# Performance work log

Hardware: AMD Instinct MI355X
Metric: run time of the kernel (lower is better)

Reference implementation:

```python
import jax, jax.numpy as jnp
import numpy as np

NE = 32          # n_events
S = 65536        # n_samples
FR = 128         # n_frames
SR = 22050       # samplerate
NRES = 1024      # n_resonances
IEXP = 8         # instr_expressivity
NEXP = 4         # noise_expressivity
NFILT = 64       # n_noise_filters
FSAMP = 512      # noise_filter_samples
NDEF = 64        # n_deformations
NNDEF = 32       # noise_deformations
NENV = 64        # n_envelopes
NDEC = 64        # n_decays
ENV_SMALL = 128  # Envelopes n_samples
ENV_FULL = 8192  # Envelopes full_size
NVERB = 16       # number of impulse responses


def interp_last(x, size):
    # linear interpolation along last axis (align_corners=True style)
    n = x.shape[-1]
    pos = jnp.linspace(0.0, n - 1.0, size)
    lo = jnp.floor(pos).astype(jnp.int32)
    hi = jnp.clip(lo + 1, 0, n - 1)
    w = (pos - lo).astype(x.dtype)
    return x[..., lo] * (1.0 - w) + x[..., hi] * w


def fft_convolve(a, b):
    # linear convolution via zero-padded FFT, keep first n samples
    n = a.shape[-1]
    A = jnp.fft.rfft(a, n=2 * n)
    B = jnp.fft.rfft(b, n=2 * n)
    return jnp.fft.irfft(A * B, n=2 * n)[..., :n]


def select_items(sel, items):
    # softmax-weighted soft lookup over item bank
    return jax.nn.softmax(sel, axis=-1) @ items


def make_waves(n_samples, n_res, sr):
    freqs = np.linspace(20.0, 4000.0, num=n_res // 4)
    t = np.arange(n_samples, dtype=np.float64) / sr
    ph = freqs[:, None] * t[None, :]               # cycles
    sine = np.sin(2 * np.pi * ph)
    saw = 2.0 * (ph % 1.0) - 1.0
    square = np.sign(sine)
    tri = 2.0 * np.abs(saw) - 1.0
    w = np.concatenate([sine, saw, square, tri], axis=0)  # (n_res, n_samples)
    return jnp.asarray(w, dtype=jnp.float32)


def setup_inputs() -> dict:
    key = jax.random.key(0)
    ks = jax.random.split(key, 16)
    u = lambda k, shp: jax.random.uniform(k, shp, minval=-0.02, maxval=0.02, dtype=jnp.float32)
    inp = {
        'res_sel': jax.random.normal(ks[0], (1, NE, IEXP, NRES), jnp.float32),
        'noise_sel': jax.random.normal(ks[1], (1, NE, NEXP, NFILT), jnp.float32),
        'env_sel': jax.random.normal(ks[2], (1, NE, NENV), jnp.float32),
        'dec_sel': jax.random.normal(ks[3], (1, NE, 1, NDEC), jnp.float32),
        'def_sel': jax.random.normal(ks[4], (1, NE, NDEF), jnp.float32),
        'noise_def_sel': jax.random.normal(ks[5], (1, NE, NNDEF), jnp.float32),
        'mix_sel': jax.random.normal(ks[6], (1, NE, 2), jnp.float32),
        'room_sel': jax.random.normal(ks[7], (1, NE, NVERB), jnp.float32),
        'amp': jax.random.uniform(ks[8], (1, NE, 1), dtype=jnp.float32),
        # learned item banks (uniform(-0.02, 0.02) init as in Lookup)
        'r_items': u(ks[9], (NRES, NRES)),
        'n_items': u(ks[10], (NFILT, FSAMP)),
        'e_items': u(ks[11], (NENV, ENV_SMALL)),
        'd_items': u(ks[12], (NDEC, 1)),
        'warp_items': u(ks[13], (NDEF, IEXP * FR)),
        'nwarp_items': u(ks[14], (NNDEF, NEXP * FR)),
        # fixed buffers
        'verbs': jax.random.normal(ks[15], (NVERB, S), jnp.float32) * 0.01,
        'waves': make_waves(S, NRES, SR),
    }
    return inp


def reference(res_sel, noise_sel, env_sel, dec_sel, def_sel, noise_def_sel,
              mix_sel, room_sel, amp, r_items, n_items, e_items, d_items,
              warp_items, nwarp_items, verbs, waves):
    # --- Envelopes: items**2, soft lookup, upsample, multiply by noise, pad ---
    env = select_items(env_sel, e_items ** 2)            # (1, NE, 128)
    env = interp_last(env, ENV_FULL)                     # (1, NE, 8192)
    noise = jax.random.uniform(jax.random.key(42), env.shape,
                               minval=-1.0, maxval=1.0, dtype=env.dtype)
    env = env * noise
    impulses = jnp.pad(env, ((0, 0), (0, 0), (0, S - ENV_FULL)))  # (1, NE, S)

    # --- SampleLookup (windowed noise filters) ---
    k = jnp.arange(FSAMP, dtype=jnp.float32)
    hamming = 0.54 - 0.46 * jnp.cos(2.0 * jnp.pi * k / (FSAMP - 1))
    nfil = select_items(noise_sel, n_items * hamming)    # (1, NE, NEXP, FSAMP)
    nfil = jnp.pad(nfil, ((0, 0), (0, 0), (0, 0), (0, S - FSAMP)))
    filt = fft_convolve(impulses[:, :, None, :], nfil)   # (1, NE, NEXP, S)

    # --- noise Deformations: softmax over channel dim, upsample ---
    nd = select_items(noise_def_sel, nwarp_items)        # (1, NE, NEXP*FR)
    nd = nd.reshape(1, NE, NEXP, FR)
    nd = jax.nn.softmax(nd, axis=2)
    nd = interp_last(nd, S)                              # (1, NE, NEXP, S)
    filtered = (filt * nd).sum(axis=2)                   # (1, NE, S)

    # --- WavetableLookup resonances ---
    res = select_items(res_sel, r_items) @ waves         # (1, NE, IEXP, S)

    # --- Decays: log-domain cumsum -> exponential envelopes ---
    d_pre = 0.5 + jax.nn.sigmoid(d_items) * 0.5          # base_resonance=0.5
    d = select_items(dec_sel, d_pre)                     # (1, NE, 1, 1)
    d = jnp.tile(d, (1, 1, 1, FR))                       # (1, NE, 1, FR)
    d = jnp.exp(jnp.cumsum(jnp.log(d + 1e-12), axis=-1))
    d = interp_last(d, S)                                # (1, NE, 1, S)

    # --- instrument Deformations ---
    w = select_items(def_sel, warp_items)                # (1, NE, IEXP*FR)
    w = w.reshape(1, NE, IEXP, FR)
    w = jax.nn.softmax(w, axis=2)
    w = interp_last(w, S)                                # (1, NE, IEXP, S)

    dres = (res * d * w).sum(axis=2)                     # (1, NE, S)

    # --- excite resonances with filtered noise, add reverb, mix ---
    conv = fft_convolve(filtered, dres)                  # (1, NE, S)
    rooms = select_items(room_sel, verbs)                # (1, NE, S)
    wet = fft_convolve(conv, rooms)
    m = jax.nn.softmax(mix_sel, axis=-1)                 # (1, NE, 2)
    mixed = m[..., 0:1] * conv + m[..., 1:2] * wet
    return mixed * (amp ** 2)                            # (1, NE, S)
```

## Files before the change

### kernel.cpp

```cpp
#include <hip/hip_runtime.h>
#include <math.h>

#define NEV    32
#define NS     65536
#define NFFT   131072
#define ENVS   128
#define ENVF   8192
#define FSAMP2 512
#define NEXP2  4
#define FLEN   8704
#define GD     5622750u
#define GDH    2811375u

enum : size_t {
  O_ENV_SMALL = 0,
  O_NFIL      = 4096,
  O_IMP       = 69632,
  O_ND        = 331776,
  O_WSM       = 348160,
  O_DSM       = 380928,
  O_SCAL      = 385024,
  O_RHO       = 385152,
  O_P1        = 385664,
  O_P2        = 647808,
// ... 275 lines not shown
    Ahi[base + (size_t)(mg*8 + r)*8] = f2bf(acc[r]);
}

__global__ __launch_bounds__(64) void prep_kernel(
    const float* __restrict__ noise_sel, const float* __restrict__ env_sel,
    const float* __restrict__ dec_sel,   const float* __restrict__ def_sel,
    const float* __restrict__ ndef_sel,  const float* __restrict__ mix_sel,
    const float* __restrict__ room_sel,  const float* __restrict__ amp,
    const float* __restrict__ n_items,   const float* __restrict__ e_items,
    const float* __restrict__ d_items,   const float* __restrict__ warp_items,
    const float* __restrict__ nwarp_items,
    float* __restrict__ env_small, float* __restrict__ nfil,
    float* __restrict__ nd_small,  float* __restrict__ w_small,
    float* __restrict__ d_small,   float* __restrict__ scal,
    float* __restrict__ rho)
{
  const int e = blockIdx.x;
  const int l = threadIdx.x;
  __shared__ float sw[64];
  __shared__ float buf[1024];

  {
    float x = env_sel[e*64 + l];
    float mx = wmax(x);
    float ex = expf(x - mx);
    float sm = wsum(ex);
    sw[l] = ex / sm;
  }
  __syncthreads();
  #pragma unroll
  for (int c = 0; c < 2; c++){
    int j = l + 64*c;
    float acc = 0.f;
    for (int k = 0; k < 64; k++){ float it = e_items[k*ENVS + j]; acc += sw[k]*(it*it); }
    env_small[e*ENVS + j] = acc;
  }
  __syncthreads();

  for (int x = 0; x < NEXP2; x++){
    float v = noise_sel[(e*NEXP2 + x)*64 + l];
    float mxv = wmax(v);
    float exv = expf(v - mxv);
    float smv = wsum(exv);
    sw[l] = exv / smv;
    __syncthreads();
    for (int c = 0; c < 8; c++){
      int tau = l + 64*c;
      float acc = 0.f;
      for (int f = 0; f < 64; f++) acc += sw[f]*n_items[f*FSAMP2 + tau];
      float ham = 0.54f - 0.46f*cosf((6.2831853071795864769f * (float)tau) / 511.0f);
      nfil[(e*NEXP2 + x)*FSAMP2 + tau] = acc*ham;
    }
    __syncthreads();
  }

  {
    float x = def_sel[e*64 + l];
    float mx = wmax(x);
    float ex = expf(x - mx);
    float sm = wsum(ex);
    sw[l] = ex / sm;
  }
  __syncthreads();
  for (int c = 0; c < 16; c++){
    int idx = l + 64*c;
    float acc = 0.f;
    for (int k = 0; k < 64; k++) acc += sw[k]*warp_items[k*1024 + idx];
    buf[idx] = acc;
  }
  __syncthreads();
  #pragma unroll
  for (int c = 0; c < 2; c++){
    int f = l + 64*c;
    float mx = -1e30f;
    for (int i = 0; i < 8; i++) mx = fmaxf(mx, buf[i*128 + f]);
    float ev[8]; float s = 0.f;
    for (int i = 0; i < 8; i++){ ev[i] = expf(buf[i*128 + f] - mx); s += ev[i]; }
    for (int i = 0; i < 8; i++) w_small[(e*8 + i)*128 + f] = ev[i]/s;
  }
  __syncthreads();

  {
    float x = (l < 32) ? ndef_sel[e*32 + l] : -1e30f;
    float mx = wmax(x);
    float ex = (l < 32) ? expf(x - mx) : 0.f;
    float sm = wsum(ex);
    sw[l] = (l < 32) ? ex/sm : 0.f;
  }
  __syncthreads();
  for (int c = 0; c < 8; c++){
    int idx = l + 64*c;
    float acc = 0.f;
    for (int k = 0; k < 32; k++) acc += sw[k]*nwarp_items[k*512 + idx];
    buf[idx] = acc;
  }
  __syncthreads();
  #pragma unroll
  for (int c = 0; c < 2; c++){
    int j = l + 64*c;
    float mx = -1e30f;
    for (int x = 0; x < 4; x++) mx = fmaxf(mx, buf[x*128 + j]);
    float ev[4]; float s = 0.f;
    for (int x = 0; x < 4; x++){ ev[x] = expf(buf[x*128 + j] - mx); s += ev[x]; }
    for (int x = 0; x < 4; x++) nd_small[(e*4 + x)*128 + j] = ev[x]/s;
  }
  __syncthreads();

  {
    float x = dec_sel[e*64 + l];
    float mx = wmax(x);
    float ex = expf(x - mx);
    float sm = wsum(ex);
    float wgt = ex / sm;
    float di = d_items[l];
    float dp = 0.5f + 0.5f*(1.0f/(1.0f + expf(-di)));
    float d0 = wsum(wgt*dp);
    float ld = logf(d0 + 1e-12f);
    #pragma unroll
    for (int c = 0; c < 2; c++){
      int f = l + 64*c;
      d_small[e*128 + f] = expf((float)(f+1)*ld);
    }
  }
  if (l == 0){
    float a = mix_sel[e*2 + 0], b = mix_sel[e*2 + 1];
    float mm = fmaxf(a, b);
    float ea = expf(a - mm), eb = expf(b - mm);
    float ss = ea + eb;
    scal[e*4 + 0] = ea/ss;
    scal[e*4 + 1] = eb/ss;
    float am = amp[e];
    scal[e*4 + 2] = am*am;
  }
  {
    float x = (l < 16) ? room_sel[e*16 + l] : -1e30f;
    float mx = wmax(x);
    float ex = (l < 16) ? expf(x - mx) : 0.f;
    float sm = wsum(ex);
    if (l < 16) rho[e*16 + l] = ex/sm;
  }
}

__global__ __launch_bounds__(256) void p1_softmax_kernel(
    const float* __restrict__ res_sel, float* __restrict__ P1)
{
  const int m = blockIdx.x;
  const int tid = threadIdx.x;
  __shared__ float red[4], red2[4];
  const float* row = res_sel + (size_t)m*1024;
  float4 v = ((const float4*)row)[tid];
  float mx = fmaxf(fmaxf(v.x, v.y), fmaxf(v.z, v.w));
  #pragma unroll
  for (int o = 32; o > 0; o >>= 1) mx = fmaxf(mx, __shfl_xor(mx, o));
  if ((tid & 63) == 0) red[tid >> 6] = mx;
  __syncthreads();
  mx = fmaxf(fmaxf(red[0], red[1]), fmaxf(red[2], red[3]));
  float e0 = expf(v.x - mx), e1 = expf(v.y - mx), e2 = expf(v.z - mx), e3 = expf(v.w - mx);
  float s = e0 + e1 + e2 + e3;
  #pragma unroll
  for (int o = 32; o > 0; o >>= 1) s += __shfl_xor(s, o);
  if ((tid & 63) == 0) red2[tid >> 6] = s;
  __syncthreads();
  s = red2[0] + red2[1] + red2[2] + red2[3];
  float inv = 1.0f/s;
  ((float4*)(P1 + (size_t)m*1024))[tid] = make_float4(e0*inv, e1*inv, e2*inv, e3*inv);
}

__global__ __launch_bounds__(256) void p2_kernel(
    const float* __restrict__ P1, const float* __restrict__ r_items,
    float* __restrict__ P2)
{
  __shared__ __align__(16) float sp1[8][1024];
  const int bx = blockIdx.x;
  const int mg = blockIdx.y;
  const int tid = threadIdx.x;
  for (int idx = tid; idx < 2048; idx += 256)
    ((float4*)&sp1[0][0])[idx] = ((const float4*)(P1 + (size_t)mg*8*1024))[idx];
  __syncthreads();
  const int n = bx*256 + tid;
  float acc[8] = {0,0,0,0,0,0,0,0};
  for (int k = 0; k < 1024; k++){
    float wv = r_items[(size_t)k*1024 + n];
    #pragma unroll
    for (int r = 0; r < 8; r++) acc[r] += sp1[r][k]*wv;
  }
  #pragma unroll
  for (int r = 0; r < 8; r++) P2[(size_t)(mg*8 + r)*1024 + n] = acc[r];
}

__global__ __launch_bounds__(256) void env_noise_kernel(
    const float* __restrict__ env_small, float* __restrict__ impulses)
{
  const int flat = blockIdx.x*256 + threadIdx.x;
  const int e = flat >> 13, i = flat & 8191;
  unsigned bits = threefry_bits(0u, (unsigned)flat);
  float u01 = __uint_as_float((bits >> 9) | 0x3f800000u) - 1.0f;
  float nz  = fmaxf(-1.0f, u01*2.0f - 1.0f);
  float pos = (float)i * (127.0f/8191.0f);
  int lo = (int)floorf(pos);
  int hi = imin(lo + 1, 127);
  float w = pos - (float)lo;
  const float* es = env_small + e*ENVS;
  float v = es[lo]*(1.0f - w) + es[hi]*w;
  impulses[flat] = v*nz;
}

__global__ __launch_bounds__(256) void filt_kernel(
    const float* __restrict__ nfil, const float* __restrict__ impulses,
    const float* __restrict__ nd_small, float* __restrict__ filtered)
{
  __shared__ float nf[4*512];
  __shared__ float imp[768];
  const int e = blockIdx.y, t0 = blockIdx.x*256, tid = threadIdx.x;
  for (int idx = tid; idx < 2048; idx += 256) nf[idx] = nfil[e*2048 + idx];
  for (int idx = tid; idx < 768; idx += 256){
    int g = t0 - 512 + idx;
    imp[idx] = (g >= 0 && g < ENVF) ? impulses[e*ENVF + g] : 0.f;
  }
  __syncthreads();
  const int t = t0 + tid;
  float s0 = 0.f, s1 = 0.f, s2 = 0.f, s3 = 0.f;
  for (int tau = 0; tau < 512; tau++){
    float iv = imp[512 + tid - tau];
    s0 += nf[0*512 + tau]*iv;
    s1 += nf[1*512 + tau]*iv;
    s2 += nf[2*512 + tau]*iv;
    s3 += nf[3*512 + tau]*iv;
  }
  float pos = (float)t * (127.0f/65535.0f);
  int lo = (int)floorf(pos);
  int hi = imin(lo + 1, 127);
  float w = pos - (float)lo;
  const float* nds = nd_small + e*512;
  float acc = 0.f;
  acc += s0*(nds[0*128 + lo]*(1.0f - w) + nds[0*128 + hi]*w);
  acc += s1*(nds[1*128 + lo]*(1.0f - w) + nds[1*128 + hi]*w);
  acc += s2*(nds[2*128 + lo]*(1.0f - w) + nds[2*128 + hi]*w);
  acc += s3*(nds[3*128 + lo]*(1.0f - w) + nds[3*128 + hi]*w);
  filtered[e*FLEN + t] = acc;
}

__global__ __launch_bounds__(256) void rooms_kernel(
    const float* __restrict__ verbs, const float* __restrict__ rho,
    float* __restrict__ rooms)
{
  const int t = blockIdx.x*256 + threadIdx.x;
  const int e = blockIdx.y;
  float acc = 0.f;
  #pragma unroll
  for (int v = 0; v < 16; v++) acc += rho[e*16 + v]*verbs[(size_t)v*NS + t];
  rooms[(size_t)e*NS + t] = acc;
}

__device__ __noinline__ float slow_wave(int wf, int n, int i){
  const double stp = 3980.0 / 255.0;
  double fi = (i == 255) ? 4000.0 : __dadd_rn(__dmul_rn((double)i, stp), 20.0);
  double tn = (double)n / 22050.0;
  double ph = __dmul_rn(fi, tn);
  double fr = ph - trunc(ph);
  if (wf == 1) return (float)(2.0*fr - 1.0);
  if (wf == 3){ double sw = 2.0*fr - 1.0; return (float)(2.0*fabs(sw) - 1.0); }
  if (fr == 0.0 || fr == 0.5){
    if (ph == 0.0) return 0.0f;
    double sv = sin(__dmul_rn(6.283185307179586, ph));
    return (sv > 0.0) ? 1.0f : ((sv < 0.0) ? -1.0f : 0.0f);
  }
  return (fr < 0.5) ? 1.0f : -1.0f;
}

__device__ __forceinline__ void gen8(int wf, int n, int i0,
                                     unsigned m_in, unsigned stepn,
                                     U8& bh, U8& bl)
{
  unsigned m = m_in;
  #pragma unroll
  for (int j = 0; j < 8; j++){
    float fr = (float)m * (1.0f/5622750.0f);
    float val;
    bool rare;
    if (wf == 0){
      asm("v_sin_f32 %0, %1" : "=v"(val) : "v"(fr));
      rare = false;
    } else if (wf == 1){
      val = fmaf(fr, 2.0f, -1.0f);
      rare = (m == 0u);
    } else if (wf == 2){
      val = (m < GDH) ? 1.0f : -1.0f;
      rare = (m == 0u) || (m == GDH);
    } else {
      val = fmaf(fabsf(fmaf(fr, 2.0f, -1.0f)), 2.0f, -1.0f);
      rare = (m == 0u);
    }
    if (rare) val = slow_wave(wf, n, i0 + j);
    unsigned ub = __float_as_uint(val);
    unsigned th = ub & 0xFFFF0000u;
    float lres = val - __uint_as_float(th);
    bh.u[j] = (unsigned short)(ub >> 16);
    bl.u[j] = (unsigned short)(__float_as_uint(lres) >> 16);
    m += stepn;
    if (m >= GD) m -= GD;
  }
}

__global__ __launch_bounds__(512, 2) void gemm_dres_gen3_kernel(
    const unsigned short* __restrict__ Ahi,
    const float* __restrict__ w_small, const float* __restrict__ d_small,
    float* __restrict__ dres)
{
  __shared__ __align__(16) unsigned short Abuf[2][8192];

  const int tid = threadIdx.x;
  const int l = tid & 63, w = tid >> 6;
  const int g = l >> 4, c = l & 15;
  const int n = blockIdx.x*128 + w*16 + c;

  f32x4 acc[16];
  #pragma unroll
  for (int m = 0; m < 16; m++) acc[m] = (f32x4){0.f,0.f,0.f,0.f};

  const unsigned stepn = (3980u*(unsigned)n) % GD;
  const unsigned s32 = (32u*stepn) % GD;
  const unsigned K0g = 3980u*(unsigned)(g*8) + 5100u;
  const unsigned m0 = (unsigned)(((unsigned long long)(unsigned)n * K0g) % GD);
  unsigned mseg = m0;

  typedef const __attribute__((address_space(1))) void GV;
  typedef __attribute__((address_space(3))) void LV;

  #pragma unroll
  for (int q = 0; q < 2; q++){
    const unsigned short* src = Ahi + (size_t)q*4096 + (size_t)w*512 + (size_t)l*8;
    __builtin_amdgcn_global_load_lds((GV*)src, (LV*)&Abuf[0][q*4096 + w*512], 16, 0, 0);
  }
  __syncthreads();

  for (int k0 = 0; k0 < 1024; k0 += 32){
    const int cur = (k0 >> 5) & 1, nxt = cur ^ 1;
    const int wf = k0 >> 8;
    if ((k0 & 255) == 0) mseg = m0;

    if (k0 + 32 < 1024){
      const size_t slice = (size_t)((k0 + 32) >> 5) * 8192;
      #pragma unroll
      for (int q = 0; q < 2; q++){
        const unsigned short* src = Ahi + slice + (size_t)q*4096 + (size_t)w*512 + (size_t)l*8;
        __builtin_amdgcn_global_load_lds((GV*)src, (LV*)&Abuf[nxt][q*4096 + w*512], 16, 0, 0);
      }
    }

    const int i0 = (k0 & 255) + g*8;
    U8 bh, bl;
    gen8(wf, n, i0, mseg, stepn, bh, bl);
    mseg += s32; if (mseg >= GD) mseg -= GD;

    #pragma unroll
    for (int m = 0; m < 16; m++){
      U8 ah;
      ah.q = *(const uint4*)&Abuf[cur][g*2048 + (m*16 + c)*8];
      acc[m] = __builtin_amdgcn_mfma_f32_16x16x32_bf16(ah.v, bh.v, acc[m], 0, 0, 0);
      acc[m] = __builtin_amdgcn_mfma_f32_16x16x32_bf16(ah.v, bl.v, acc[m], 0, 0, 0);
    }
    __syncthreads();
  }

  const int t = n;
  float pos = (float)t * (127.0f/65535.0f);
  int lo = (int)floorf(pos);
  int hi = imin(lo + 1, 127);
  float fr = pos - (float)lo;
  #pragma unroll
  for (int m = 0; m < 16; m++){
    int e = 2*m + (g >> 1);
    float s = 0.f;
    #pragma unroll
    for (int jj = 0; jj < 4; jj++){
      int i = (g & 1)*4 + jj;
      const float* wr = w_small + (size_t)(e*8 + i)*128;
      float wi = wr[lo]*(1.0f - fr) + wr[hi]*fr;
      s += wi * acc[m][jj];
    }
    s += __shfl_xor(s, 16);
    if ((g & 1) == 0){
      float de = d_small[e*128 + lo]*(1.0f - fr) + d_small[e*128 + hi]*fr;
      dres[(size_t)e*NS + t] = de * s;
    }
  }
}

__global__ __launch_bounds__(256) void gemm_dres_kernel(
    const float* __restrict__ P2, const float* __restrict__ waves,
    const float* __restrict__ w_small, const float* __restrict__ d_small,
    float* __restrict__ dres)
{
  __shared__ __align__(16) float At[32][256];
  __shared__ __align__(16) float Bt[32][64];
  const int tid = threadIdx.x;
  const int tx = tid & 15, ty = tid >> 4;
  const int n0 = blockIdx.x * 64;
  float acc[16][4];
  #pragma unroll
  for (int a = 0; a < 16; a++)
    #pragma unroll
    for (int b = 0; b < 4; b++) acc[a][b] = 0.f;

  for (int k0 = 0; k0 < 1024; k0 += 32){
    {
      const float4* src = (const float4*)(P2 + (size_t)tid*1024 + k0);
      #pragma unroll
      for (int q = 0; q < 8; q++){
        float4 v = src[q];
        At[q*4 + 0][tid] = v.x; At[q*4 + 1][tid] = v.y;
        At[q*4 + 2][tid] = v.z; At[q*4 + 3][tid] = v.w;
      }
    }
    {
      int c  = tid & 15;
      int kr = tid >> 4;
      *(float4*)&Bt[kr][c*4]      = *((const float4*)(waves + (size_t)(k0 + kr)*NS + n0) + c);
      *(float4*)&Bt[kr + 16][c*4] = *((const float4*)(waves + (size_t)(k0 + kr + 16)*NS + n0) + c);
    }
    __syncthreads();
    #pragma unroll 4
    for (int k = 0; k < 32; k++){
      float a[16];
      *(float4*)&a[0]  = *(const float4*)&At[k][ty*16 + 0];
      *(float4*)&a[4]  = *(const float4*)&At[k][ty*16 + 4];
      *(float4*)&a[8]  = *(const float4*)&At[k][ty*16 + 8];
      *(float4*)&a[12] = *(const float4*)&At[k][ty*16 + 12];
      float4 b = *(const float4*)&Bt[k][tx*4];
      #pragma unroll
      for (int mi = 0; mi < 16; mi++){
        acc[mi][0] += a[mi]*b.x;
        acc[mi][1] += a[mi]*b.y;
        acc[mi][2] += a[mi]*b.z;
        acc[mi][3] += a[mi]*b.w;
      }
    }
    __syncthreads();
  }

  #pragma unroll
  for (int ni = 0; ni < 4; ni++){
    int t = n0 + tx*4 + ni;
    float pos = (float)t * (127.0f/65535.0f);
    int lo = (int)floorf(pos);
    int hi = imin(lo + 1, 127);
    float w = pos - (float)lo;
    #pragma unroll
    for (int ev2 = 0; ev2 < 2; ev2++){
      int e = ty*2 + ev2;
      float de = d_small[e*128 + lo]*(1.0f - w) + d_small[e*128 + hi]*w;
      float s = 0.f;
      #pragma unroll
      for (int i = 0; i < 8; i++){
        const float* wrow = w_small + (size_t)(e*8 + i)*128;
        float wi = wrow[lo]*(1.0f - w) + wrow[hi]*w;
        s += wi * acc[ev2*8 + i][ni];
      }
      dres[(size_t)e*NS + t] = de * s;
    }
  }
}


template<int L, int Ns, int DIR>
__device__ __forceinline__ void r4_stage(const float* __restrict__ xr,
                                         const float* __restrict__ xi,
                                         float* __restrict__ yr,
                                         float* __restrict__ yi)
{
  const int tid = threadIdx.x;
  constexpr int BPR = L/4;
  #pragma unroll
  for (int q = 0; q < 4; q++){
    int bf = tid + 256*q;
    int r  = bf / BPR;
    int j  = bf % BPR;
    int sw = (r & 7) << 2;
    int jm = j & (Ns - 1);
    float2 w1 = twid((float)jm * (1.0f/(4.0f*(float)Ns)));
    if (DIR < 0) w1.y = -w1.y;
    float2 w2 = make_float2(w1.x*w1.x - w1.y*w1.y, 2.0f*w1.x*w1.y);
    float2 w3 = make_float2(w2.x*w1.x - w2.y*w1.y, w2.x*w1.y + w2.y*w1.x);
    const float* xrr = xr + r*L;
    const float* xir = xi + r*L;
    float ar  = xrr[j ^ sw],           ai  = xir[j ^ sw];
    float b0r = xrr[(j+BPR) ^ sw],     b0i = xir[(j+BPR) ^ sw];
    float c0r = xrr[(j+2*BPR) ^ sw],   c0i = xir[(j+2*BPR) ^ sw];
    float d0r = xrr[(j+3*BPR) ^ sw],   d0i = xir[(j+3*BPR) ^ sw];
    float br = b0r*w1.x - b0i*w1.y,  bi = b0r*w1.y + b0i*w1.x;
    float cr = c0r*w2.x - c0i*w2.y,  ci = c0r*w2.y + c0i*w2.x;
    float dr = d0r*w3.x - d0i*w3.y,  di = d0r*w3.y + d0i*w3.x;
    float apc_r = ar + cr, apc_i = ai + ci;
    float amc_r = ar - cr, amc_i = ai - ci;
    float bpd_r = br + dr, bpd_i = bi + di;
    float bmd_r = br - dr, bmd_i = bi - di;
    int dbase = ((j - jm) << 2) + jm;
    float* yrr = yr + r*L;
    float* yir = yi + r*L;
    yrr[dbase ^ sw]          = apc_r + bpd_r;
    yir[dbase ^ sw]          = apc_i + bpd_i;
    yrr[(dbase + 2*Ns) ^ sw] = apc_r - bpd_r;
    yir[(dbase + 2*Ns) ^ sw] = apc_i - bpd_i;
    if (DIR > 0){
      yrr[(dbase + Ns) ^ sw]   = amc_r + bmd_i;
      yir[(dbase + Ns) ^ sw]   = amc_i - bmd_r;
      yrr[(dbase + 3*Ns) ^ sw] = amc_r - bmd_i;
      yir[(dbase + 3*Ns) ^ sw] = amc_i + bmd_r;
    } else {
      yrr[(dbase + Ns) ^ sw]   = amc_r - bmd_i;
      yir[(dbase + Ns) ^ sw]   = amc_i + bmd_r;
      yrr[(dbase + 3*Ns) ^ sw] = amc_r + bmd_i;
      yir[(dbase + 3*Ns) ^ sw] = amc_i - bmd_r;
    }
  }
}

#define FFT_SWAP { float* t_; t_=ra;ra=rb;rb=t_; t_=ia;ia=ib;ib=t_; }

template<int L, int DIR>
__device__ __forceinline__ void fft_core4(float*& ra, float*& ia, float*& rb, float*& ib)
{
  const int tid = threadIdx.x;
  if (L == 512){
    __syncthreads();
    #pragma unroll
    for (int q = 0; q < 8; q++){
      int bf = tid + 256*q;
      int r = bf >> 8, j = bf & 255;
      int sw = (r & 7) << 2;
      float ar = ra[r*512 + (j ^ sw)],        ai = ia[r*512 + (j ^ sw)];
      float br = ra[r*512 + ((j+256) ^ sw)],  bi = ia[r*512 + ((j+256) ^ sw)];
      rb[r*512 + ((2*j) ^ sw)]   = ar + br;
      ib[r*512 + ((2*j) ^ sw)]   = ai + bi;
      rb[r*512 + ((2*j+1) ^ sw)] = ar - br;
      ib[r*512 + ((2*j+1) ^ sw)] = ai - bi;
    }
    FFT_SWAP
    __syncthreads(); r4_stage<512,   2, DIR>(ra, ia, rb, ib); FFT_SWAP
    __syncthreads(); r4_stage<512,   8, DIR>(ra, ia, rb, ib); FFT_SWAP
    __syncthreads(); r4_stage<512,  32, DIR>(ra, ia, rb, ib); FFT_SWAP
    __syncthreads(); r4_stage<512, 128, DIR>(ra, ia, rb, ib); FFT_SWAP
  } else {
    __syncthreads(); r4_stage<256,   1, DIR>(ra, ia, rb, ib); FFT_SWAP
    __syncthreads(); r4_stage<256,   4, DIR>(ra, ia, rb, ib); FFT_SWAP
    __syncthreads(); r4_stage<256,  16, DIR>(ra, ia, rb, ib); FFT_SWAP
    __syncthreads(); r4_stage<256,  64, DIR>(ra, ia, rb, ib); FFT_SWAP
  }
  __syncthreads();
}

__global__ __launch_bounds__(256) void fwd512_all_kernel(
    const float* __restrict__ filt, const float* __restrict__ dresv,
    const float* __restrict__ verbs, const float* __restrict__ rho,
    float2* __restrict__ Xf, float2* __restrict__ Xd, float2* __restrict__ Xr)
{
  __shared__ float reA[4096], imA[4096], reB[4096], imB[4096];
  __shared__ float srho[32];
  const int e = blockIdx.y, t1 = blockIdx.x*8, tid = threadIdx.x;
  const int z = blockIdx.z;
  if (z == 2){
    if (tid < 32) srho[tid] = rho[(2*e)*16 + tid];
    __syncthreads();
  }
  #pragma unroll
  for (int q = 0; q < 4; q++){
    int flat = tid + 256*q;
    int n2 = flat >> 1;
    int rb = (flat & 1)*4;
    int nb = t1 + rb + 256*n2;
    float4 va = make_float4(0.f,0.f,0.f,0.f);
    float4 vb = make_float4(0.f,0.f,0.f,0.f);
    if (z == 0){
      if (nb < FLEN){
        va = *(const float4*)(filt + (size_t)e*2*FLEN + nb);
        vb = *(const float4*)(filt + (size_t)e*2*FLEN + FLEN + nb);
      }
    } else if (z == 1){
      if (nb < NS){
        va = *(const float4*)(dresv + (size_t)e*2*NS + nb);
        vb = *(const float4*)(dresv + (size_t)e*2*NS + NS + nb);
      }
    } else {
      if (nb < NS){
        #pragma unroll
        for (int v = 0; v < 16; v++){
          float4 w4 = *(const float4*)(verbs + (size_t)v*NS + nb);
          float r0 = srho[v], r1 = srho[16 + v];
          va.x += r0*w4.x; va.y += r0*w4.y; va.z += r0*w4.z; va.w += r0*w4.w;
          vb.x += r1*w4.x; vb.y += r1*w4.y; vb.z += r1*w4.z; vb.w += r1*w4.w;
        }
      }
    }
    #pragma unroll
    for (int j = 0; j < 4; j++){
      int r = rb + j;
      int sw = (r & 7) << 2;
      reA[r*512 + (n2 ^ sw)] = (&va.x)[j];
      imA[r*512 + (n2 ^ sw)] = (&vb.x)[j];
    }
  }
  float *ra = reA, *ia = imA, *rb2 = reB, *ib2 = imB;
  fft_core4<512, +1>(ra, ia, rb2, ib2);
  float2* Bt = (z == 0) ? Xf : (z == 1) ? Xd : Xr;
  float2* dst = Bt + ((size_t)e << 17);
  #pragma unroll
  for (int q = 0; q < 16; q++){
    int idx = tid + 256*q;
    int r = idx & 7, k2 = idx >> 3;
    int n1 = t1 + r;
    int sw = (r & 7) << 2;
    float xr = ra[r*512 + (k2 ^ sw)];
    float xi = ia[r*512 + (k2 ^ sw)];
    float2 w = twid((float)(n1*k2) * (1.0f/131072.0f));
    dst[k2*256 + n1] = make_float2(xr*w.x - xi*w.y, xr*w.y + xi*w.x);
  }
}

__device__ __forceinline__ void fwd256_body(float2* __restrict__ S)
{
  __shared__ float reA[4096], imA[4096], reB[4096], imB[4096];
  const int e = blockIdx.y, K0 = blockIdx.x*16, tid = threadIdx.x;
  float2* base = S + ((size_t)e << 17) + (size_t)K0*256;
  #pragma unroll
  for (int q = 0; q < 16; q++){
    int idx = tid + 256*q;
    int r = idx >> 8, col = idx & 255;
    float2 v = base[r*256 + col];
    int sw = (r & 7) << 2;
    reA[r*256 + (col ^ sw)] = v.x;
    imA[r*256 + (col ^ sw)] = v.y;
  }
  float *ra = reA, *ia = imA, *rb = reB, *ib = imB;
  fft_core4<256, +1>(ra, ia, rb, ib);
  #pragma unroll
  for (int q = 0; q < 16; q++){
    int idx = tid + 256*q;
    int r = idx >> 8, col = idx & 255;
    int sw = (r & 7) << 2;
    base[r*256 + col] = make_float2(ra[r*256 + (col ^ sw)], ia[r*256 + (col ^ sw)]);
  }
}

__global__ __launch_bounds__(256) void fwd256_tri_kernel(
    float2* __restrict__ Xf, float2* __restrict__ Xd, float2* __restrict__ Xr)
{
  float2* S = (blockIdx.z == 0) ? Xf : (blockIdx.z == 1) ? Xd : Xr;
  fwd256_body(S);
}

__global__ __launch_bounds__(256) void fwd256_kernel(float2* __restrict__ S)
{
  fwd256_body(S);
}

__global__ __launch_bounds__(256) void inv256_mul2_kernel(
    const float2* __restrict__ ZA, const float2* __restrict__ ZB,
    float2* __restrict__ Ut)
{
  __shared__ float reA[4096], imA[4096], reB[4096], imB[4096];
  const int e = blockIdx.y, K0 = blockIdx.x*16, tid = threadIdx.x;
  const float2* Za = ZA + ((size_t)e << 17);
  const float2* Zb = ZB + ((size_t)e << 17);
  #pragma unroll
  for (int q = 0; q < 16; q++){
    int idx = tid + 256*q;
    int r = idx >> 8, col = idx & 255;
    int k2 = K0 + r;
    int k2p, k1p;
    if (k2 == 0){ k2p = 0; k1p = (256 - col) & 255; }
    else        { k2p = 512 - k2; k1p = 255 - col; }
    float2 za  = Za[(size_t)k2*256 + col];
    float2 zap = Za[(size_t)k2p*256 + k1p];
    float2 zb  = Zb[(size_t)k2*256 + col];
    float2 zbp = Zb[(size_t)k2p*256 + k1p];
    float a0r = 0.5f*(za.x + zap.x), a0i = 0.5f*(za.y - zap.y);
    float a1r = 0.5f*(za.y + zap.y), a1i = 0.5f*(zap.x - za.x);
    float b0r = 0.5f*(zb.x + zbp.x), b0i = 0.5f*(zb.y - zbp.y);
    float b1r = 0.5f*(zb.y + zbp.y), b1i = 0.5f*(zbp.x - zb.x);
    float p0r = a0r*b0r - a0i*b0i, p0i = a0r*b0i + a0i*b0r;
    float p1r = a1r*b1r - a1i*b1i, p1i = a1r*b1i + a1i*b1r;
    int sw = (r & 7) << 2;
    reA[r*256 + (col ^ sw)] = p0r - p1i;
    imA[r*256 + (col ^ sw)] = p0i + p1r;
  }
  float *ra = reA, *ia = imA, *rb = reB, *ib = imB;
  fft_core4<256, -1>(ra, ia, rb, ib);
  float2* dst = Ut + ((size_t)e << 17);
  #pragma unroll
  for (int q = 0; q < 16; q++){
    int idx = tid + 256*q;
    int r = idx & 15, n1 = idx >> 4;
    int k2 = K0 + r;
    int sw = (r & 7) << 2;
    float xr = ra[r*256 + (n1 ^ sw)];
    float xi = ia[r*256 + (n1 ^ sw)];
    float2 w = twid((float)(n1*k2) * (1.0f/131072.0f));
    dst[n1*512 + k2] = make_float2(xr*w.x + xi*w.y, xi*w.x - xr*w.y);
  }
}

__global__ __launch_bounds__(256) void inv512_fwdpack2_kernel(
    const float2* __restrict__ Ut, float* __restrict__ conv,
    float2* __restrict__ Bt)
{
  __shared__ float reA[4096], imA[4096], reB[4096], imB[4096];
  const int e = blockIdx.y, t1 = blockIdx.x*8, tid = threadIdx.x;
  const float2* base = Ut + ((size_t)e << 17) + (size_t)t1*512;
  #pragma unroll
  for (int q = 0; q < 16; q++){
    int idx = tid + 256*q;
    int r = idx >> 9, col = idx & 511;
    float2 v = base[r*512 + col];
    int sw = (r & 7) << 2;
    reA[r*512 + (col ^ sw)] = v.x;
    imA[r*512 + (col ^ sw)] = v.y;
  }
  float *ra = reA, *ia = imA, *rb = reB, *ib = imB;
  fft_core4<512, -1>(ra, ia, rb, ib);
  const float s = 1.0f/131072.0f;
  #pragma unroll
  for (int q = 0; q < 16; q++){
    int idx = tid + 256*q;
    int r = idx & 7, n2 = idx >> 3;
    int sw = (r & 7) << 2;
    int pos = r*512 + (n2 ^ sw);
    if (n2 < 256){
      int n = (t1 + r) + 256*n2;
      float y0 = ra[pos]*s, y1 = ia[pos]*s;
      conv[(size_t)(2*e)*NS + n]     = y0;
      conv[(size_t)(2*e + 1)*NS + n] = y1;
      rb[pos] = y0; ib[pos] = y1;
    } else {
      rb[pos] = 0.f; ib[pos] = 0.f;
    }
  }
  __syncthreads();
  float *r2 = rb, *i2 = ib, *r3 = ra, *i3 = ia;
  fft_core4<512, +1>(r2, i2, r3, i3);
  float2* dst = Bt + ((size_t)e << 17);
  #pragma unroll
  for (int q = 0; q < 16; q++){
    int idx = tid + 256*q;
    int r = idx & 7, k2 = idx >> 3;
    int n1 = t1 + r;
    int sw = (r & 7) << 2;
    float xr = r2[r*512 + (k2 ^ sw)];
    float xi = i2[r*512 + (k2 ^ sw)];
    float2 w = twid((float)(n1*k2) * (1.0f/131072.0f));
    dst[k2*256 + n1] = make_float2(xr*w.x - xi*w.y, xr*w.y + xi*w.x);
  }
}

__global__ __launch_bounds__(256) void inv512_mix2_kernel(
    const float2* __restrict__ Ut, const float* __restrict__ conv,
    const float* __restrict__ scal, float* __restrict__ dst)
{
  __shared__ float reA[4096], imA[4096], reB[4096], imB[4096];
  const int e = blockIdx.y, t1 = blockIdx.x*8, tid = threadIdx.x;
  const float2* base = Ut + ((size_t)e << 17) + (size_t)t1*512;
  #pragma unroll
  for (int q = 0; q < 16; q++){
    int idx = tid + 256*q;
    int r = idx >> 9, col = idx & 511;
    float2 v = base[r*512 + col];
    int sw = (r & 7) << 2;
    reA[r*512 + (col ^ sw)] = v.x;
    imA[r*512 + (col ^ sw)] = v.y;
  }
  float *ra = reA, *ia = imA, *rb = reB, *ib = imB;
  fft_core4<512, -1>(ra, ia, rb, ib);
  const float s = 1.0f/131072.0f;
  const int e0 = 2*e, e1 = 2*e + 1;
  float m00 = scal[e0*4 + 0], m10 = scal[e0*4 + 1], a20 = scal[e0*4 + 2];
  float m01 = scal[e1*4 + 0], m11 = scal[e1*4 + 1], a21 = scal[e1*4 + 2];
  #pragma unroll
  for (int q = 0; q < 8; q++){
    int idx = tid + 256*q;
    int r = idx & 7, n2 = idx >> 3;
    int n = (t1 + r) + 256*n2;
    int sw = (r & 7) << 2;
    int pos = r*512 + (n2 ^ sw);
    float w0 = ra[pos]*s, w1 = ia[pos]*s;
    size_t g0 = (size_t)e0*NS + n, g1 = (size_t)e1*NS + n;
    dst[g0] = (m00*conv[g0] + m10*w0)*a20;
    dst[g1] = (m01*conv[g1] + m11*w1)*a21;
  }
}

template<int MODE>
__global__ __launch_bounds__(256) void tconv_kernel(
    const float* __restrict__ sig, int sig_len, int sig_stride,
    const float* __restrict__ go, const float* __restrict__ scal,
    float* __restrict__ dst)
{
  __shared__ __align__(16) float cs[2048];
  __shared__ __align__(16) float rs[4104];
  const int e = blockIdx.y;
  const int t0 = blockIdx.x * 2048;
  const int tid = threadIdx.x;
  const int tb = tid * 8;
  float acc[8] = {0,0,0,0,0,0,0,0};
  const int kcap = imin(sig_len, t0 + 2048);
  for (int c0 = 0; c0 < kcap; c0 += 2048){
    __syncthreads();
    for (int idx = tid; idx < 2048; idx += 256){
      int gsi = c0 + idx;
      cs[idx] = (gsi < sig_len) ? sig[(size_t)e*sig_stride + gsi] : 0.f;
    }
    const int rb = t0 - c0 - 2056;
    for (int idx = tid; idx < 4104; idx += 256){
      int g = rb + idx;
      rs[idx] = (g >= 0 && g < NS) ? go[(size_t)e*NS + g] : 0.f;
    }
    __syncthreads();
    float W[12];
    int P = tb + 2056;
    *(float4*)&W[0] = *(const float4*)&rs[P - 4];
    *(float4*)&W[4] = *(const float4*)&rs[P];
    *(float4*)&W[8] = *(const float4*)&rs[P + 4];
    for (int u = 0; u < 512; u++){
      float4 f4 = *(const float4*)&cs[4*u];
      #pragma unroll
      for (int j = 0; j < 8; j++){
        acc[j] += f4.x*W[4 + j];
        acc[j] += f4.y*W[3 + j];
        acc[j] += f4.z*W[2 + j];
        acc[j] += f4.w*W[1 + j];
      }
      #pragma unroll
      for (int x2 = 11; x2 >= 4; x2--) W[x2] = W[x2 - 4];
      P -= 4;
      *(float4*)&W[0] = *(const float4*)&rs[P - 4];
    }
  }
  if (MODE == 0){
    #pragma unroll
    for (int j = 0; j < 8; j++) dst[(size_t)e*NS + t0 + tb + j] = acc[j];
  } else {
    float m0 = scal[e*4 + 0], m1 = scal[e*4 + 1], a2 = scal[e*4 + 2];
    #pragma unroll
    for (int j = 0; j < 8; j++){
      size_t gi = (size_t)e*NS + t0 + tb + j;
      dst[gi] = (m0*sig[gi] + m1*acc[j]) * a2;
    }
  }
}

extern "C" void kernel_launch(void* const* d_in, const int* in_sizes, int n_in,
                              void* d_out, int out_size, void* d_ws, size_t ws_size,
                              hipStream_t stream)
{
  (void)in_sizes; (void)n_in; (void)out_size;
  const float* res_sel     = (const float*)d_in[0];
  const float* noise_sel   = (const float*)d_in[1];
  const float* env_sel     = (const float*)d_in[2];
  const float* dec_sel     = (const float*)d_in[3];
  const float* def_sel     = (const float*)d_in[4];
  const float* ndef_sel    = (const float*)d_in[5];
  const float* mix_sel     = (const float*)d_in[6];
  const float* room_sel    = (const float*)d_in[7];
  const float* amp         = (const float*)d_in[8];
  const float* r_items     = (const float*)d_in[9];
  const float* n_items     = (const float*)d_in[10];
  const float* e_items     = (const float*)d_in[11];
  const float* d_items     = (const float*)d_in[12];
  const float* warp_items  = (const float*)d_in[13];
  const float* nwarp_items = (const float*)d_in[14];
  const float* verbs       = (const float*)d_in[15];
  const float* waves       = (const float*)d_in[16];
  float* ws  = (float*)d_ws;
  float* out = (float*)d_out;

  const bool big_ws = ws_size >= (size_t)O_END * sizeof(float);

  if (big_ws) {
    weights_kernel<<<dim3(NEV), dim3(64), 0, stream>>>(
        noise_sel, env_sel, dec_sel, def_sel, ndef_sel, mix_sel, room_sel, amp,
        d_items, ws + O_SWE, ws + O_SWN, ws + O_SWD, ws + O_SWND,
        ws + O_DSM, ws + O_SCAL, ws + O_RHO);
    lookups_kernel<<<dim3(224), dim3(256), 0, stream>>>(
        ws + O_SWE, ws + O_SWN, ws + O_SWD, ws + O_SWND,
        e_items, n_items, warp_items, nwarp_items,
        ws + O_ENV_SMALL, ws + O_NFIL, ws + O_WSM, ws + O_ND);

    unsigned short* Ahi = (unsigned short*)(ws + O_X);
    p2s_kernel<<<dim3(4, 32), dim3(256), 0, stream>>>(res_sel, r_items, Ahi);

    env_noise_kernel<<<dim3(1024), dim3(256), 0, stream>>>(ws + O_ENV_SMALL, ws + O_IMP);
    filt_kernel<<<dim3(34, NEV), dim3(256), 0, stream>>>(ws + O_NFIL, ws + O_IMP, ws + O_ND, ws + O_FILT);

    gemm_dres_gen3_kernel<<<dim3(512), dim3(512), 0, stream>>>(
        Ahi, ws + O_WSM, ws + O_DSM, ws + O_DRES);

    float2* Xf = (float2*)(ws + O_X);
    float2* Xd = (float2*)(ws + O_X + 4194304);
    float2* Xr = (float2*)(ws + O_Y);
    float2* Uc = (float2*)(ws + O_Y + 4194304);
    float2* Xc = Xf;
    float2* Uw = Xd;

    fwd512_all_kernel<<<dim3(32, 16, 3), dim3(256), 0, stream>>>(
        ws + O_FILT, ws + O_DRES, verbs, ws + O_RHO, Xf, Xd, Xr);
    fwd256_tri_kernel<<<dim3(32, 16, 3), dim3(256), 0, stream>>>(Xf, Xd, Xr);

    inv256_mul2_kernel<<<dim3(32, 16), dim3(256), 0, stream>>>(Xf, Xd, Uc);
    inv512_fwdpack2_kernel<<<dim3(32, 16), dim3(256), 0, stream>>>(Uc, ws + O_CONV, Xc);
    fwd256_kernel<<<dim3(32, 16), dim3(256), 0, stream>>>(Xc);
    inv256_mul2_kernel<<<dim3(32, 16), dim3(256), 0, stream>>>(Xc, Xr, Uw);
    inv512_mix2_kernel<<<dim3(32, 16), dim3(256), 0, stream>>>(
        Uw, ws + O_CONV, ws + O_SCAL, out);
  } else {
    prep_kernel<<<dim3(NEV), dim3(64), 0, stream>>>(
        noise_sel, env_sel, dec_sel, def_sel, ndef_sel, mix_sel, room_sel, amp,
        n_items, e_items, d_items, warp_items, nwarp_items,
        ws + O_ENV_SMALL, ws + O_NFIL, ws + O_ND, ws + O_WSM,
        ws + O_DSM, ws + O_SCAL, ws + O_RHO);
    p1_softmax_kernel<<<dim3(256), dim3(256), 0, stream>>>(res_sel, ws + O_P1);
    p2_kernel<<<dim3(4, 32), dim3(256), 0, stream>>>(ws + O_P1, r_items, ws + O_P2);
    env_noise_kernel<<<dim3(1024), dim3(256), 0, stream>>>(ws + O_ENV_SMALL, ws + O_IMP);
    filt_kernel<<<dim3(34, NEV), dim3(256), 0, stream>>>(ws + O_NFIL, ws + O_IMP, ws + O_ND, ws + O_FILT);
    rooms_kernel<<<dim3(256, NEV), dim3(256), 0, stream>>>(verbs, ws + O_RHO, ws + O_ROOMS);
    gemm_dres_kernel<<<dim3(1024), dim3(256), 0, stream>>>(
        ws + O_P2, waves, ws + O_WSM, ws + O_DSM, ws + O_DRES);
    tconv_kernel<0><<<dim3(32, NEV), dim3(256), 0, stream>>>(
        ws + O_FILT, FLEN, FLEN, ws + O_DRES, (const float*)nullptr, ws + O_CONV);
    tconv_kernel<1><<<dim3(32, NEV), dim3(256), 0, stream>>>(
        ws + O_CONV, NS, NS, ws + O_ROOMS, ws + O_SCAL, out);
  }
}
```

Baseline: 356.2 us.

## Fold dry/wet mix into spectral multiply and double GEMM K-step per stage

```diff
diff --git a/kernel.cpp b/kernel.cpp
--- a/kernel.cpp
+++ b/kernel.cpp
@@ -601,12 +601,12 @@
   }
 }
 
-__global__ __launch_bounds__(512, 2) void gemm_dres_gen3_kernel(
+__global__ __launch_bounds__(512, 2) void gemm_dres_gen4_kernel(
     const unsigned short* __restrict__ Ahi,
     const float* __restrict__ w_small, const float* __restrict__ d_small,
     float* __restrict__ dres)
 {
-  __shared__ __align__(16) unsigned short Abuf[2][8192];
+  __shared__ __align__(16) unsigned short Abuf[2][16384];
 
   const int tid = threadIdx.x;
   const int l = tid & 63, w = tid >> 6;
@@ -627,37 +627,40 @@
   typedef __attribute__((address_space(3))) void LV;
 
   #pragma unroll
-  for (int q = 0; q < 2; q++){
+  for (int q = 0; q < 4; q++){
     const unsigned short* src = Ahi + (size_t)q*4096 + (size_t)w*512 + (size_t)l*8;
     __builtin_amdgcn_global_load_lds((GV*)src, (LV*)&Abuf[0][q*4096 + w*512], 16, 0, 0);
   }
   __syncthreads();
 
-  for (int k0 = 0; k0 < 1024; k0 += 32){
-    const int cur = (k0 >> 5) & 1, nxt = cur ^ 1;
+  for (int k0 = 0; k0 < 1024; k0 += 64){
+    const int cur = (k0 >> 6) & 1, nxt = cur ^ 1;
     const int wf = k0 >> 8;
     if ((k0 & 255) == 0) mseg = m0;
 
-    if (k0 + 32 < 1024){
-      const size_t slice = (size_t)((k0 + 32) >> 5) * 8192;
+    if (k0 + 64 < 1024){
+      const size_t sb = (size_t)((k0 + 64) >> 5) * 8192;
       #pragma unroll
-      for (int q = 0; q < 2; q++){
-        const unsigned short* src = Ahi + slice + (size_t)q*4096 + (size_t)w*512 + (size_t)l*8;
+      for (int q = 0; q < 4; q++){
+        const unsigned short* src = Ahi + sb + (size_t)q*4096 + (size_t)w*512 + (size_t)l*8;
         __builtin_amdgcn_global_load_lds((GV*)src, (LV*)&Abuf[nxt][q*4096 + w*512], 16, 0, 0);
       }
     }
 
-    const int i0 = (k0 & 255) + g*8;
-    U8 bh, bl;
-    gen8(wf, n, i0, mseg, stepn, bh, bl);
-    mseg += s32; if (mseg >= GD) mseg -= GD;
-
-    #pragma unroll
-    for (int m = 0; m < 16; m++){
-      U8 ah;
-      ah.q = *(const uint4*)&Abuf[cur][g*2048 + (m*16 + c)*8];
-      acc[m] = __builtin_amdgcn_mfma_f32_16x16x32_bf16(ah.v, bh.v, acc[m], 0, 0, 0);
-      acc[m] = __builtin_amdgcn_mfma_f32_16x16x32_bf16(ah.v, bl.v, acc[m], 0, 0, 0);
+    #pragma unroll
+    for (int ks = 0; ks < 2; ks++){
+      const int i0 = (k0 & 255) + 32*ks + g*8;
+      U8 bh, bl;
+      gen8(wf, n, i0, mseg, stepn, bh, bl);
+      mseg += s32; if (mseg >= GD) mseg -= GD;
+      const int abase = ks*8192 + g*2048;
+      #pragma unroll
+      for (int m = 0; m < 16; m++){
+        U8 ah;
+        ah.q = *(const uint4*)&Abuf[cur][abase + (m*16 + c)*8];
+        acc[m] = __builtin_amdgcn_mfma_f32_16x16x32_bf16(ah.v, bh.v, acc[m], 0, 0, 0);
+        acc[m] = __builtin_amdgcn_mfma_f32_16x16x32_bf16(ah.v, bl.v, acc[m], 0, 0, 0);
+      }
     }
     __syncthreads();
   }
@@ -999,9 +1002,58 @@
   }
 }
 
+__global__ __launch_bounds__(256) void inv256_mulmix_kernel(
+    const float2* __restrict__ ZA, const float2* __restrict__ ZB,
+    const float* __restrict__ scal, float2* __restrict__ Ut)
+{
+  __shared__ float reA[4096], imA[4096], reB[4096], imB[4096];
+  const int e = blockIdx.y, K0 = blockIdx.x*16, tid = threadIdx.x;
+  const float2* Za = ZA + ((size_t)e << 17);
+  const float2* Zb = ZB + ((size_t)e << 17);
+  const float m00 = scal[(2*e)*4 + 0], m10 = scal[(2*e)*4 + 1];
+  const float m01 = scal[(2*e+1)*4 + 0], m11 = scal[(2*e+1)*4 + 1];
+  #pragma unroll
+  for (int q = 0; q < 16; q++){
+    int idx = tid + 256*q;
+    int r = idx >> 8, col = idx & 255;
+    int k2 = K0 + r;
+    int k2p, k1p;
+    if (k2 == 0){ k2p = 0; k1p = (256 - col) & 255; }
+    else        { k2p = 512 - k2; k1p = 255 - col; }
+    float2 za  = Za[(size_t)k2*256 + col];
+    float2 zap = Za[(size_t)k2p*256 + k1p];
+    float2 zb  = Zb[(size_t)k2*256 + col];
+    float2 zbp = Zb[(size_t)k2p*256 + k1p];
+    float a0r = 0.5f*(za.x + zap.x), a0i = 0.5f*(za.y - zap.y);
+    float a1r = 0.5f*(za.y + zap.y), a1i = 0.5f*(zap.x - za.x);
+    float b0r = 0.5f*(zb.x + zbp.x), b0i = 0.5f*(zb.y - zbp.y);
+    float b1r = 0.5f*(zb.y + zbp.y), b1i = 0.5f*(zbp.x - zb.x);
+    float B0r = m00 + m10*b0r, B0i = m10*b0i;
+    float B1r = m01 + m11*b1r, B1i = m11*b1i;
+    float p0r = a0r*B0r - a0i*B0i, p0i = a0r*B0i + a0i*B0r;
+    float p1r = a1r*B1r - a1i*B1i, p1i = a1r*B1i + a1i*B1r;
+    int sw = (r & 7) << 2;
+    reA[r*256 + (col ^ sw)] = p0r - p1i;
+    imA[r*256 + (col ^ sw)] = p0i + p1r;
+  }
+  float *ra = reA, *ia = imA, *rb = reB, *ib = imB;
+  fft_core4<256, -1>(ra, ia, rb, ib);
+  float2* dst = Ut + ((size_t)e << 17);
+  #pragma unroll
+  for (int q = 0; q < 16; q++){
+    int idx = tid + 256*q;
+    int r = idx & 15, n1 = idx >> 4;
+    int k2 = K0 + r;
+    int sw = (r & 7) << 2;
+    float xr = ra[r*256 + (n1 ^ sw)];
+    float xi = ia[r*256 + (n1 ^ sw)];
+    float2 w = twid((float)(n1*k2) * (1.0f/131072.0f));
+    dst[n1*512 + k2] = make_float2(xr*w.x + xi*w.y, xi*w.x - xr*w.y);
+  }
+}
+
 __global__ __launch_bounds__(256) void inv512_fwdpack2_kernel(
-    const float2* __restrict__ Ut, float* __restrict__ conv,
-    float2* __restrict__ Bt)
+    const float2* __restrict__ Ut, float2* __restrict__ Bt)
 {
   __shared__ float reA[4096], imA[4096], reB[4096], imB[4096];
   const int e = blockIdx.y, t1 = blockIdx.x*8, tid = threadIdx.x;
@@ -1025,11 +1077,7 @@
     int sw = (r & 7) << 2;
     int pos = r*512 + (n2 ^ sw);
     if (n2 < 256){
-      int n = (t1 + r) + 256*n2;
-      float y0 = ra[pos]*s, y1 = ia[pos]*s;
-      conv[(size_t)(2*e)*NS + n]     = y0;
-      conv[(size_t)(2*e + 1)*NS + n] = y1;
-      rb[pos] = y0; ib[pos] = y1;
+      rb[pos] = ra[pos]*s; ib[pos] = ia[pos]*s;
     } else {
       rb[pos] = 0.f; ib[pos] = 0.f;
     }
@@ -1051,9 +1099,9 @@
   }
 }
 
-__global__ __launch_bounds__(256) void inv512_mix2_kernel(
-    const float2* __restrict__ Ut, const float* __restrict__ conv,
-    const float* __restrict__ scal, float* __restrict__ dst)
+__global__ __launch_bounds__(256) void inv512_out_kernel(
+    const float2* __restrict__ Ut, const float* __restrict__ scal,
+    float* __restrict__ dst)
 {
   __shared__ float reA[4096], imA[4096], reB[4096], imB[4096];
   const int e = blockIdx.y, t1 = blockIdx.x*8, tid = threadIdx.x;
@@ -1071,8 +1119,7 @@
   fft_core4<512, -1>(ra, ia, rb, ib);
   const float s = 1.0f/131072.0f;
   const int e0 = 2*e, e1 = 2*e + 1;
-  float m00 = scal[e0*4 + 0], m10 = scal[e0*4 + 1], a20 = scal[e0*4 + 2];
-  float m01 = scal[e1*4 + 0], m11 = scal[e1*4 + 1], a21 = scal[e1*4 + 2];
+  const float a20 = scal[e0*4 + 2]*s, a21 = scal[e1*4 + 2]*s;
   #pragma unroll
   for (int q = 0; q < 8; q++){
     int idx = tid + 256*q;
@@ -1080,10 +1127,8 @@
     int n = (t1 + r) + 256*n2;
     int sw = (r & 7) << 2;
     int pos = r*512 + (n2 ^ sw);
-    float w0 = ra[pos]*s, w1 = ia[pos]*s;
-    size_t g0 = (size_t)e0*NS + n, g1 = (size_t)e1*NS + n;
-    dst[g0] = (m00*conv[g0] + m10*w0)*a20;
-    dst[g1] = (m01*conv[g1] + m11*w1)*a21;
+    dst[(size_t)e0*NS + n] = ra[pos]*a20;
+    dst[(size_t)e1*NS + n] = ia[pos]*a21;
   }
 }
 
@@ -1189,7 +1234,7 @@
     env_noise_kernel<<<dim3(1024), dim3(256), 0, stream>>>(ws + O_ENV_SMALL, ws + O_IMP);
     filt_kernel<<<dim3(34, NEV), dim3(256), 0, stream>>>(ws + O_NFIL, ws + O_IMP, ws + O_ND, ws + O_FILT);
 
-    gemm_dres_gen3_kernel<<<dim3(512), dim3(512), 0, stream>>>(
+    gemm_dres_gen4_kernel<<<dim3(512), dim3(512), 0, stream>>>(
         Ahi, ws + O_WSM, ws + O_DSM, ws + O_DRES);
 
     float2* Xf = (float2*)(ws + O_X);
@@ -1204,11 +1249,10 @@
     fwd256_tri_kernel<<<dim3(32, 16, 3), dim3(256), 0, stream>>>(Xf, Xd, Xr);
 
     inv256_mul2_kernel<<<dim3(32, 16), dim3(256), 0, stream>>>(Xf, Xd, Uc);
-    inv512_fwdpack2_kernel<<<dim3(32, 16), dim3(256), 0, stream>>>(Uc, ws + O_CONV, Xc);
+    inv512_fwdpack2_kernel<<<dim3(32, 16), dim3(256), 0, stream>>>(Uc, Xc);
     fwd256_kernel<<<dim3(32, 16), dim3(256), 0, stream>>>(Xc);
-    inv256_mul2_kernel<<<dim3(32, 16), dim3(256), 0, stream>>>(Xc, Xr, Uw);
-    inv512_mix2_kernel<<<dim3(32, 16), dim3(256), 0, stream>>>(
-        Uw, ws + O_CONV, ws + O_SCAL, out);
+    inv256_mulmix_kernel<<<dim3(32, 16), dim3(256), 0, stream>>>(Xc, Xr, ws + O_SCAL, Uw);
+    inv512_out_kernel<<<dim3(32, 16), dim3(256), 0, stream>>>(Uw, ws + O_SCAL, out);
   } else {
     prep_kernel<<<dim3(NEV), dim3(64), 0, stream>>>(
         noise_sel, env_sel, dec_sel, def_sel, ndef_sel, mix_sel, room_sel, amp,
```

Result: no change. 349.6 us (-1.8%).
